# Kernel optimization log

Measured on AMD Instinct MI355X. Metric: run time of the kernel, lower is better.

Reference implementation:

```python
import jax, jax.numpy as jnp
import numpy as np

N_NODES = 50000
N_EDGES = 800000
IN_DIM = 100
HIDDEN = 16
N_CLASSES = 40


def setup_inputs() -> dict:
    key = jax.random.key(0)
    k1, k2, k3, k4, k5, k6 = jax.random.split(key, 6)
    features = jax.random.normal(k1, (N_NODES, IN_DIM), dtype=jnp.float32)
    edge_src = jax.random.randint(k2, (N_EDGES,), 0, N_NODES, dtype=jnp.int32)
    edge_dst = jax.random.randint(k3, (N_EDGES,), 0, N_NODES, dtype=jnp.int32)
    edge_vals = jax.random.uniform(k4, (N_EDGES,), dtype=jnp.float32)
    W1 = jax.random.uniform(k5, (IN_DIM, HIDDEN), dtype=jnp.float32)
    W2 = jax.random.uniform(k6, (HIDDEN, N_CLASSES), dtype=jnp.float32)
    return {"features": features, "edge_src": edge_src, "edge_dst": edge_dst,
            "edge_vals": edge_vals, "W1": W1, "W2": W2}


def _spmm(edge_src, edge_dst, edge_vals, x):
    # z = A @ x with A given as (dst, src, val) edge list; equivalent to the
    # partition-loop addmm accumulation in broadcast().
    msgs = edge_vals[:, None] * x[edge_src]            # [E, d]
    return jax.ops.segment_sum(msgs, edge_dst, num_segments=x.shape[0])


def reference(features, edge_src, edge_dst, edge_vals, W1, W2):
    h = jax.nn.relu(_spmm(edge_src, edge_dst, edge_vals, features) @ W1)  # [N, 16]
    out = _spmm(edge_src, edge_dst, edge_vals, h) @ W2                    # [N, C]
    return jax.nn.log_softmax(out, axis=1)
```

## Files before the change

### kernel.cpp

```cpp
#include <hip/hip_runtime.h>

#define N_NODES   50000
#define N_EDGES   800000
#define IN_DIM    100
#define HIDDEN    16
#define N_CLASSES 40

#define BSHIFT 6
#define NPB    64
#define NBKT   782
#define PB     256
#define EPB    3125
#define CAP    2048
#define GNODES 32

#define GROWS 64
__global__ __launch_bounds__(256) void gemm_xw1(const float* __restrict__ X,
                                                const float* __restrict__ W,
                                                float* __restrict__ Y) {
    __shared__ __align__(16) float sX[GROWS * IN_DIM];
    __shared__ __align__(16) float sW[IN_DIM * HIDDEN];
    const int tid  = threadIdx.x;
    const int row0 = blockIdx.x * GROWS;
    const int nrows = min(GROWS, N_NODES - row0);

    const float4* W4 = (const float4*)W;
    float4* sW4 = (float4*)sW;
    for (int i = tid; i < (IN_DIM * HIDDEN) / 4; i += 256) sW4[i] = W4[i];

    const float4* X4 = (const float4*)(X + (size_t)row0 * IN_DIM);
    float4* sX4 = (float4*)sX;
    const int nf4 = nrows * (IN_DIM / 4);
    for (int i = tid; i < nf4; i += 256) sX4[i] = X4[i];
    __syncthreads();

    const int r = tid >> 2;
    const int q = tid & 3;
    if (r >= nrows) return;

    float4 acc = make_float4(0.f, 0.f, 0.f, 0.f);
    const float* xr = &sX[r * IN_DIM];
#pragma unroll
    for (int k = 0; k < IN_DIM; ++k) {
        const float xk = xr[k];
        const float4 w = *(const float4*)&sW[k * HIDDEN + q * 4];
        acc.x = fmaf(xk, w.x, acc.x);
        acc.y = fmaf(xk, w.y, acc.y);
        acc.z = fmaf(xk, w.z, acc.z);
        acc.w = fmaf(xk, w.w, acc.w);
    }
    *(float4*)&Y[(size_t)(row0 + r) * HIDDEN + q * 4] = acc;
}

__global__ __launch_bounds__(512) void partition_kernel(const int* __restrict__ src,
                                                        const int* __restrict__ dst,
                                                        const float* __restrict__ val,
                                                        int* __restrict__ BTt,
                                                        int2* __restrict__ binned) {
    __shared__ int  cnt[NBKT];
    __shared__ int  lcur[NBKT];
    __shared__ int  sd[512];
    __shared__ int2 staged[EPB];

    const int tid = threadIdx.x, b = blockIdx.x;
    const int e0 = b * EPB;

    for (int k = tid; k < NBKT; k += 512) cnt[k] = 0;
    __syncthreads();
    for (int i = tid; i < EPB; i += 512)
        atomicAdd(&cnt[dst[e0 + i] >> BSHIFT], 1);
    __syncthreads();

    const int k0 = 2 * tid, k1 = 2 * tid + 1;
    const int a  = (k0 < NBKT) ? cnt[k0] : 0;
    const int bb = (k1 < NBKT) ? cnt[k1] : 0;
    const int s  = a + bb;
    sd[tid] = s;
    __syncthreads();
    for (int off = 1; off < 512; off <<= 1) {
        const int u = (tid >= off) ? sd[tid - off] : 0;
        __syncthreads();
        sd[tid] += u;
        __syncthreads();
    }
    const int excl = sd[tid] - s;
    if (k0 < NBKT) { lcur[k0] = excl;     BTt[k0 * PB + b] = excl; }
    if (k1 < NBKT) { lcur[k1] = excl + a; BTt[k1 * PB + b] = excl + a; }
    if (tid == 0)  BTt[NBKT * PB + b] = EPB;
    __syncthreads();

    for (int i = tid; i < EPB; i += 512) {
        const int e = e0 + i;
        const int d = dst[e];
        const int k = d >> BSHIFT;
        const int pos = atomicAdd(&lcur[k], 1);
        staged[pos] = make_int2(src[e] | ((d & (NPB - 1)) << 16),
                                __float_as_int(val[e]));
    }
    __syncthreads();

    for (int i = tid; i < EPB; i += 512)
        binned[e0 + i] = staged[i];
}

__global__ __launch_bounds__(256) void sort_kernel(const int* __restrict__ BTt,
                                                   const int2* __restrict__ binned,
                                                   int2* __restrict__ sorted,
                                                   int2* __restrict__ meta) {
    __shared__ int  cnt[NPB];
    __shared__ int  cur[NPB];
    __shared__ int  sTot;
    __shared__ int2 staged[CAP];

    const int tid = threadIdx.x, k = blockIdx.x;
    if (tid < NPB) cnt[tid] = 0;
    __syncthreads();

    const int rs = BTt[k * PB + tid];
    const int re = BTt[(k + 1) * PB + tid];
    const int2* rb = binned + (size_t)tid * EPB;

    for (int p = rs; p < re; ++p)
        atomicAdd(&cnt[(rb[p].x >> 16) & (NPB - 1)], 1);
    __syncthreads();

    if (tid < NPB) {
        const int v  = cnt[tid];
        const int vp = (v + 1) & ~1;
        int x = vp;
#pragma unroll
        for (int d = 1; d < 64; d <<= 1) {
            const int y = __shfl_up(x, d, 64);
            if (tid >= d) x += y;
        }
        const int excl = x - vp;
        cur[tid] = excl;
        const int node = k * NPB + tid;
        if (node < N_NODES) meta[node] = make_int2(k * CAP + excl, v);
        if (tid == NPB - 1) sTot = x;
    }
    __syncthreads();

    for (int p = rs; p < re; ++p) {
        const int2 e = rb[p];
        const int  n = (e.x >> 16) & (NPB - 1);
        const int pos = atomicAdd(&cur[n], 1);
        staged[pos] = make_int2(e.x & 0xFFFF, e.y);
    }
    __syncthreads();

    const int m = sTot;
    for (int i = tid; i < m; i += 256)
        sorted[(size_t)k * CAP + i] = staged[i];
}

template <bool RELU_OUT>
__global__ __launch_bounds__(256) void gather_spmm(const int2* __restrict__ meta,
                                                   const int2* __restrict__ sorted,
                                                   const float* __restrict__ X,
                                                   float* __restrict__ Z) {
    const int tid = threadIdx.x;
    const int g = tid >> 3, j = tid & 7;
    const int n = blockIdx.x * GNODES + g;
    if (n >= N_NODES) return;
    const int2 md = meta[n];
    const int beg = md.x, end = md.x + md.y;
    const float2* X2 = (const float2*)X;

    float2 acc = make_float2(0.f, 0.f);
    int p = beg;
    for (; p + 4 <= end; p += 4) {
        const int4 ea = *(const int4*)&sorted[p];
        const int4 eb = *(const int4*)&sorted[p + 2];
        const float2 x0 = X2[(size_t)ea.x * 8 + j];
        const float2 x1 = X2[(size_t)ea.z * 8 + j];
        const float2 x2 = X2[(size_t)eb.x * 8 + j];
        const float2 x3 = X2[(size_t)eb.z * 8 + j];
        const float v0 = __int_as_float(ea.y), v1 = __int_as_float(ea.w);
        const float v2 = __int_as_float(eb.y), v3 = __int_as_float(eb.w);
        acc.x = fmaf(v0, x0.x, acc.x); acc.y = fmaf(v0, x0.y, acc.y);
        acc.x = fmaf(v1, x1.x, acc.x); acc.y = fmaf(v1, x1.y, acc.y);
        acc.x = fmaf(v2, x2.x, acc.x); acc.y = fmaf(v2, x2.y, acc.y);
        acc.x = fmaf(v3, x3.x, acc.x); acc.y = fmaf(v3, x3.y, acc.y);
    }
    for (; p < end; ++p) {
        const int2 e = sorted[p];
        const float2 x = X2[(size_t)e.x * 8 + j];
        const float v = __int_as_float(e.y);
        acc.x = fmaf(v, x.x, acc.x); acc.y = fmaf(v, x.y, acc.y);
    }
    if (RELU_OUT) { acc.x = fmaxf(acc.x, 0.f); acc.y = fmaxf(acc.y, 0.f); }
    ((float2*)Z)[(size_t)n * 8 + j] = acc;
}

__global__ __launch_bounds__(256) void gather_out(const int2* __restrict__ meta,
                                                  const int2* __restrict__ sorted,
                                                  const float* __restrict__ X,
                                                  const float* __restrict__ W2,
                                                  float* __restrict__ out) {
    __shared__ float sW[HIDDEN * N_CLASSES];
    __shared__ float zt[GNODES * 17];
    const int tid = threadIdx.x;
    for (int i = tid; i < HIDDEN * N_CLASSES; i += 256) sW[i] = W2[i];

    const int g = tid >> 3, j = tid & 7;
    const int n = blockIdx.x * GNODES + g;

    float2 acc = make_float2(0.f, 0.f);
    if (n < N_NODES) {
        const int2 md = meta[n];
        const int beg = md.x, end = md.x + md.y;
        const float2* X2 = (const float2*)X;
        int p = beg;
        for (; p + 4 <= end; p += 4) {
            const int4 ea = *(const int4*)&sorted[p];
            const int4 eb = *(const int4*)&sorted[p + 2];
            const float2 x0 = X2[(size_t)ea.x * 8 + j];
            const float2 x1 = X2[(size_t)ea.z * 8 + j];
            const float2 x2 = X2[(size_t)eb.x * 8 + j];
            const float2 x3 = X2[(size_t)eb.z * 8 + j];
            const float v0 = __int_as_float(ea.y), v1 = __int_as_float(ea.w);
            const float v2 = __int_as_float(eb.y), v3 = __int_as_float(eb.w);
            acc.x = fmaf(v0, x0.x, acc.x); acc.y = fmaf(v0, x0.y, acc.y);
            acc.x = fmaf(v1, x1.x, acc.x); acc.y = fmaf(v1, x1.y, acc.y);
            acc.x = fmaf(v2, x2.x, acc.x); acc.y = fmaf(v2, x2.y, acc.y);
            acc.x = fmaf(v3, x3.x, acc.x); acc.y = fmaf(v3, x3.y, acc.y);
        }
        for (; p < end; ++p) {
            const int2 e = sorted[p];
            const float2 x = X2[(size_t)e.x * 8 + j];
            const float v = __int_as_float(e.y);
            acc.x = fmaf(v, x.x, acc.x); acc.y = fmaf(v, x.y, acc.y);
        }
    }
    zt[g * 17 + j * 2]     = acc.x;
    zt[g * 17 + j * 2 + 1] = acc.y;
    __syncthreads();
    if (n >= N_NODES) return;

    float z[HIDDEN];
#pragma unroll
    for (int k = 0; k < HIDDEN; ++k) z[k] = zt[g * 17 + k];

    float o[5];
#pragma unroll
    for (int i = 0; i < 5; ++i) o[i] = 0.f;
#pragma unroll
    for (int k = 0; k < HIDDEN; ++k) {
        const float zk = z[k];
#pragma unroll
        for (int i = 0; i < 5; ++i)
            o[i] = fmaf(zk, sW[k * N_CLASSES + j * 5 + i], o[i]);
    }

    float m = o[0];
#pragma unroll
    for (int i = 1; i < 5; ++i) m = fmaxf(m, o[i]);
#pragma unroll
    for (int d = 1; d < 8; d <<= 1) m = fmaxf(m, __shfl_xor(m, d, 8));
    float se = 0.f;
#pragma unroll
    for (int i = 0; i < 5; ++i) se += __expf(o[i] - m);
#pragma unroll
    for (int d = 1; d < 8; d <<= 1) se += __shfl_xor(se, d, 8);
    const float lse = m + __logf(se);

    float* orow = out + (size_t)n * N_CLASSES + j * 5;
#pragma unroll
    for (int i = 0; i < 5; ++i) orow[i] = o[i] - lse;
}

extern "C" void kernel_launch(void* const* d_in, const int* in_sizes, int n_in,
                              void* d_out, int out_size, void* d_ws, size_t ws_size,
                              hipStream_t stream) {
    const float* features = (const float*)d_in[0];
    const int*   edge_src = (const int*)d_in[1];
    const int*   edge_dst = (const int*)d_in[2];
    const float* edge_val = (const float*)d_in[3];
    const float* W1       = (const float*)d_in[4];
    const float* W2       = (const float*)d_in[5];
    float*       out      = (float*)d_out;

    char* base = (char*)d_ws;
    const size_t HNB = (size_t)N_NODES * HIDDEN * sizeof(float);
    float* y1     = (float*)(base);
    float* z1     = (float*)(base + HNB);
    int2*  binned = (int2*) (base + 2 * HNB);
    int2*  sortd  = (int2*) (base + 2 * HNB + (size_t)N_EDGES * 8);
    char*  tail   = base + 2 * HNB + (size_t)N_EDGES * 8
                         + (size_t)NBKT * CAP * 8;
    int*   BTt    = (int*) (tail);
    int2*  meta   = (int2*)(tail + (((size_t)(NBKT + 1) * PB * 4 + 255) & ~255ULL));

    partition_kernel<<<PB, 512, 0, stream>>>(edge_src, edge_dst, edge_val, BTt, binned);
    sort_kernel<<<NBKT, 256, 0, stream>>>(BTt, binned, sortd, meta);

    gemm_xw1<<<(N_NODES + GROWS - 1) / GROWS, 256, 0, stream>>>(features, W1, y1);
    gather_spmm<true><<<(N_NODES + GNODES - 1) / GNODES, 256, 0, stream>>>(meta, sortd, y1, z1);
    gather_out<<<(N_NODES + GNODES - 1) / GNODES, 256, 0, stream>>>(meta, sortd, z1, W2, out);
}
```

Baseline: 139.1 us.

## Fuse partition with XW1 GEMM and sort with first SpMM gather

Merges the edge partition and the X·W1 GEMM into one launch by splitting the grid into partition blocks and GEMM blocks, and merges the per-bucket sort with the first aggregation so it reads sorted edges straight from LDS. The partition pass now keeps edges in registers so dst/src/val are read from global memory once instead of twice. The sort kernel first copies its bucket's edges into LDS using a block-wide scan, then does counting and scattering there. This cuts five launches to three and removes a global round trip of the sorted edges, at the cost of heavier LDS use per block and one-thread-per-quarter-row gathers with unbalanced degrees.

New measurement: 125.6 us. 1.11x faster.

```diff
diff --git a/kernel.cpp b/kernel.cpp
--- a/kernel.cpp
+++ b/kernel.cpp
@@ -11,186 +11,196 @@
 #define NBKT   782
 #define PB     256
 #define EPB    3125
+#define EPT    7
 #define CAP    2048
 #define GNODES 32
-
-#define GROWS 64
-__global__ __launch_bounds__(256) void gemm_xw1(const float* __restrict__ X,
-                                                const float* __restrict__ W,
-                                                float* __restrict__ Y) {
-    __shared__ __align__(16) float sX[GROWS * IN_DIM];
-    __shared__ __align__(16) float sW[IN_DIM * HIDDEN];
-    const int tid  = threadIdx.x;
-    const int row0 = blockIdx.x * GROWS;
-    const int nrows = min(GROWS, N_NODES - row0);
-
-    const float4* W4 = (const float4*)W;
-    float4* sW4 = (float4*)sW;
-    for (int i = tid; i < (IN_DIM * HIDDEN) / 4; i += 256) sW4[i] = W4[i];
-
-    const float4* X4 = (const float4*)(X + (size_t)row0 * IN_DIM);
-    float4* sX4 = (float4*)sX;
-    const int nf4 = nrows * (IN_DIM / 4);
-    for (int i = tid; i < nf4; i += 256) sX4[i] = X4[i];
-    __syncthreads();
-
-    const int r = tid >> 2;
-    const int q = tid & 3;
-    if (r >= nrows) return;
-
-    float4 acc = make_float4(0.f, 0.f, 0.f, 0.f);
-    const float* xr = &sX[r * IN_DIM];
-#pragma unroll
-    for (int k = 0; k < IN_DIM; ++k) {
-        const float xk = xr[k];
-        const float4 w = *(const float4*)&sW[k * HIDDEN + q * 4];
-        acc.x = fmaf(xk, w.x, acc.x);
-        acc.y = fmaf(xk, w.y, acc.y);
-        acc.z = fmaf(xk, w.z, acc.z);
-        acc.w = fmaf(xk, w.w, acc.w);
-    }
-    *(float4*)&Y[(size_t)(row0 + r) * HIDDEN + q * 4] = acc;
+#define GEMMB  782
+
+#define K1_LDS 33456
+
+__global__ __launch_bounds__(512) void build_and_gemm(const int* __restrict__ src,
+                                                      const int* __restrict__ dst,
+                                                      const float* __restrict__ val,
+                                                      const float* __restrict__ X,
+                                                      const float* __restrict__ W,
+                                                      int* __restrict__ BTt,
+                                                      int2* __restrict__ binned,
+                                                      float* __restrict__ Y) {
+    __shared__ __align__(16) char smem[K1_LDS];
+    const int tid = threadIdx.x;
+
+    if (blockIdx.x < PB) {
+        int*  cnt    = (int*)smem;
+        int*  lcur   = (int*)(smem + 3200);
+        int*  sd     = (int*)(smem + 6400);
+        int2* staged = (int2*)(smem + 8448);
+        const int b = blockIdx.x, e0 = b * EPB;
+
+        for (int k = tid; k < NBKT; k += 512) cnt[k] = 0;
+        __syncthreads();
+
+        int pk[EPT], ps[EPT]; float pv[EPT];
+#pragma unroll
+        for (int q = 0; q < EPT; ++q) {
+            const int i = tid + q * 512;
+            if (i < EPB) {
+                const int e = e0 + i;
+                const int d = dst[e];
+                pk[q] = d >> BSHIFT;
+                ps[q] = src[e] | ((d & (NPB - 1)) << 16);
+                pv[q] = val[e];
+                atomicAdd(&cnt[pk[q]], 1);
+            } else pk[q] = -1;
+        }
+        __syncthreads();
+
+        const int k0 = 2 * tid, k1 = 2 * tid + 1;
+        const int a  = (k0 < NBKT) ? cnt[k0] : 0;
+        const int bb = (k1 < NBKT) ? cnt[k1] : 0;
+        const int s  = a + bb;
+        sd[tid] = s;
+        __syncthreads();
+        for (int off = 1; off < 512; off <<= 1) {
+            const int u = (tid >= off) ? sd[tid - off] : 0;
+            __syncthreads();
+            sd[tid] += u;
+            __syncthreads();
+        }
+        const int excl = sd[tid] - s;
+        if (k0 < NBKT) { lcur[k0] = excl;     BTt[k0 * PB + b] = excl; }
+        if (k1 < NBKT) { lcur[k1] = excl + a; BTt[k1 * PB + b] = excl + a; }
+        if (tid == 0)  BTt[NBKT * PB + b] = EPB;
+        __syncthreads();
+
+#pragma unroll
+        for (int q = 0; q < EPT; ++q) {
+            if (pk[q] >= 0) {
+                const int pos = atomicAdd(&lcur[pk[q]], 1);
+                staged[pos] = make_int2(ps[q], __float_as_int(pv[q]));
+            }
+        }
+        __syncthreads();
+
+        for (int i = tid; i < EPB; i += 512)
+            binned[e0 + i] = staged[i];
+    } else {
+        float* sX = (float*)smem;
+        float* sW = (float*)(smem + 25600);
+        const int b2   = blockIdx.x - PB;
+        const int row0 = b2 * 64;
+        const int nrows = min(64, N_NODES - row0);
+
+        const float4* W4 = (const float4*)W;
+        float4* sW4 = (float4*)sW;
+        for (int i = tid; i < (IN_DIM * HIDDEN) / 4; i += 512) sW4[i] = W4[i];
+        const float4* X4 = (const float4*)(X + (size_t)row0 * IN_DIM);
+        float4* sX4 = (float4*)sX;
+        const int nf4 = nrows * (IN_DIM / 4);
+        for (int i = tid; i < nf4; i += 512) sX4[i] = X4[i];
+        __syncthreads();
+
+        const int r = tid >> 3, hh = tid & 7;
+        if (r >= nrows) return;
+        float2 acc = make_float2(0.f, 0.f);
+        const float* xr = &sX[r * IN_DIM];
+#pragma unroll
+        for (int k = 0; k < IN_DIM; ++k) {
+            const float xk = xr[k];
+            const float2 w = *(const float2*)&sW[k * HIDDEN + hh * 2];
+            acc.x = fmaf(xk, w.x, acc.x);
+            acc.y = fmaf(xk, w.y, acc.y);
+        }
+        *(float2*)&Y[(size_t)(row0 + r) * HIDDEN + hh * 2] = acc;
+    }
 }
 
-__global__ __launch_bounds__(512) void partition_kernel(const int* __restrict__ src,
-                                                        const int* __restrict__ dst,
-                                                        const float* __restrict__ val,
-                                                        int* __restrict__ BTt,
-                                                        int2* __restrict__ binned) {
-    __shared__ int  cnt[NBKT];
-    __shared__ int  lcur[NBKT];
-    __shared__ int  sd[512];
-    __shared__ int2 staged[EPB];
-
-    const int tid = threadIdx.x, b = blockIdx.x;
-    const int e0 = b * EPB;
-
-    for (int k = tid; k < NBKT; k += 512) cnt[k] = 0;
-    __syncthreads();
-    for (int i = tid; i < EPB; i += 512)
-        atomicAdd(&cnt[dst[e0 + i] >> BSHIFT], 1);
-    __syncthreads();
-
-    const int k0 = 2 * tid, k1 = 2 * tid + 1;
-    const int a  = (k0 < NBKT) ? cnt[k0] : 0;
-    const int bb = (k1 < NBKT) ? cnt[k1] : 0;
-    const int s  = a + bb;
-    sd[tid] = s;
-    __syncthreads();
-    for (int off = 1; off < 512; off <<= 1) {
-        const int u = (tid >= off) ? sd[tid - off] : 0;
-        __syncthreads();
-        sd[tid] += u;
-        __syncthreads();
-    }
-    const int excl = sd[tid] - s;
-    if (k0 < NBKT) { lcur[k0] = excl;     BTt[k0 * PB + b] = excl; }
-    if (k1 < NBKT) { lcur[k1] = excl + a; BTt[k1 * PB + b] = excl + a; }
-    if (tid == 0)  BTt[NBKT * PB + b] = EPB;
-    __syncthreads();
-
-    for (int i = tid; i < EPB; i += 512) {
-        const int e = e0 + i;
-        const int d = dst[e];
-        const int k = d >> BSHIFT;
-        const int pos = atomicAdd(&lcur[k], 1);
-        staged[pos] = make_int2(src[e] | ((d & (NPB - 1)) << 16),
-                                __float_as_int(val[e]));
-    }
-    __syncthreads();
-
-    for (int i = tid; i < EPB; i += 512)
-        binned[e0 + i] = staged[i];
-}
-
-__global__ __launch_bounds__(256) void sort_kernel(const int* __restrict__ BTt,
+__global__ __launch_bounds__(256) void sort_gather(const int* __restrict__ BTt,
                                                    const int2* __restrict__ binned,
+                                                   const float* __restrict__ Xin,
                                                    int2* __restrict__ sorted,
-                                                   int2* __restrict__ meta) {
+                                                   int2* __restrict__ meta,
+                                                   float* __restrict__ Z) {
+    __shared__ int2 raw[CAP];
+    __shared__ int2 srt[CAP];
     __shared__ int  cnt[NPB];
     __shared__ int  cur[NPB];
-    __shared__ int  sTot;
-    __shared__ int2 staged[CAP];
-
+    __shared__ int  wsum[4];
     const int tid = threadIdx.x, k = blockIdx.x;
+    const int lane = tid & 63, w = tid >> 6;
+
     if (tid < NPB) cnt[tid] = 0;
-    __syncthreads();
 
     const int rs = BTt[k * PB + tid];
     const int re = BTt[(k + 1) * PB + tid];
+    const int len = re - rs;
+    int x = len;
+#pragma unroll
+    for (int d = 1; d < 64; d <<= 1) {
+        const int y = __shfl_up(x, d, 64);
+        if (lane >= d) x += y;
+    }
+    if (lane == 63) wsum[w] = x;
+    __syncthreads();
+    int add = 0;
+    for (int i = 0; i < w; ++i) add += wsum[i];
+    const int tot = wsum[0] + wsum[1] + wsum[2] + wsum[3];
+
+    int o = add + x - len;
     const int2* rb = binned + (size_t)tid * EPB;
-
-    for (int p = rs; p < re; ++p)
-        atomicAdd(&cnt[(rb[p].x >> 16) & (NPB - 1)], 1);
+    for (int p = rs; p < re; ++p, ++o) raw[o] = rb[p];
+    __syncthreads();
+
+    for (int i = tid; i < tot; i += 256)
+        atomicAdd(&cnt[(raw[i].x >> 16) & (NPB - 1)], 1);
     __syncthreads();
 
     if (tid < NPB) {
         const int v  = cnt[tid];
         const int vp = (v + 1) & ~1;
-        int x = vp;
+        int xx = vp;
 #pragma unroll
         for (int d = 1; d < 64; d <<= 1) {
-            const int y = __shfl_up(x, d, 64);
-            if (tid >= d) x += y;
-        }
-        const int excl = x - vp;
+            const int y = __shfl_up(xx, d, 64);
+            if (tid >= d) xx += y;
+        }
+        const int excl = xx - vp;
         cur[tid] = excl;
         const int node = k * NPB + tid;
         if (node < N_NODES) meta[node] = make_int2(k * CAP + excl, v);
-        if (tid == NPB - 1) sTot = x;
-    }
-    __syncthreads();
-
-    for (int p = rs; p < re; ++p) {
-        const int2 e = rb[p];
-        const int  n = (e.x >> 16) & (NPB - 1);
-        const int pos = atomicAdd(&cur[n], 1);
-        staged[pos] = make_int2(e.x & 0xFFFF, e.y);
-    }
-    __syncthreads();
-
-    const int m = sTot;
-    for (int i = tid; i < m; i += 256)
-        sorted[(size_t)k * CAP + i] = staged[i];
-}
-
-template <bool RELU_OUT>
-__global__ __launch_bounds__(256) void gather_spmm(const int2* __restrict__ meta,
-                                                   const int2* __restrict__ sorted,
-                                                   const float* __restrict__ X,
-                                                   float* __restrict__ Z) {
-    const int tid = threadIdx.x;
-    const int g = tid >> 3, j = tid & 7;
-    const int n = blockIdx.x * GNODES + g;
-    if (n >= N_NODES) return;
-    const int2 md = meta[n];
-    const int beg = md.x, end = md.x + md.y;
-    const float2* X2 = (const float2*)X;
-
-    float2 acc = make_float2(0.f, 0.f);
-    int p = beg;
-    for (; p + 4 <= end; p += 4) {
-        const int4 ea = *(const int4*)&sorted[p];
-        const int4 eb = *(const int4*)&sorted[p + 2];
-        const float2 x0 = X2[(size_t)ea.x * 8 + j];
-        const float2 x1 = X2[(size_t)ea.z * 8 + j];
-        const float2 x2 = X2[(size_t)eb.x * 8 + j];
-        const float2 x3 = X2[(size_t)eb.z * 8 + j];
-        const float v0 = __int_as_float(ea.y), v1 = __int_as_float(ea.w);
-        const float v2 = __int_as_float(eb.y), v3 = __int_as_float(eb.w);
-        acc.x = fmaf(v0, x0.x, acc.x); acc.y = fmaf(v0, x0.y, acc.y);
-        acc.x = fmaf(v1, x1.x, acc.x); acc.y = fmaf(v1, x1.y, acc.y);
-        acc.x = fmaf(v2, x2.x, acc.x); acc.y = fmaf(v2, x2.y, acc.y);
-        acc.x = fmaf(v3, x3.x, acc.x); acc.y = fmaf(v3, x3.y, acc.y);
-    }
-    for (; p < end; ++p) {
-        const int2 e = sorted[p];
-        const float2 x = X2[(size_t)e.x * 8 + j];
+        if (tid == NPB - 1) wsum[0] = xx;
+    }
+    __syncthreads();
+    const int padTot = wsum[0];
+
+    for (int i = tid; i < tot; i += 256) {
+        const int2 e = raw[i];
+        const int pos = atomicAdd(&cur[(e.x >> 16) & (NPB - 1)], 1);
+        srt[pos] = make_int2(e.x & 0xFFFF, e.y);
+    }
+    __syncthreads();
+
+    for (int i = tid; i < padTot; i += 256)
+        sorted[(size_t)k * CAP + i] = srt[i];
+
+    const int g = tid >> 2, q = tid & 3;
+    const int node = k * NPB + g;
+    if (node >= N_NODES) return;
+    const int deg = cnt[g];
+    const int beg = cur[g] - deg;
+    const float4* X4 = (const float4*)Xin;
+    float4 acc = make_float4(0.f, 0.f, 0.f, 0.f);
+    for (int p = beg; p < beg + deg; ++p) {
+        const int2 e = srt[p];
         const float v = __int_as_float(e.y);
-        acc.x = fmaf(v, x.x, acc.x); acc.y = fmaf(v, x.y, acc.y);
-    }
-    if (RELU_OUT) { acc.x = fmaxf(acc.x, 0.f); acc.y = fmaxf(acc.y, 0.f); }
-    ((float2*)Z)[(size_t)n * 8 + j] = acc;
+        const float4 xv = X4[(size_t)e.x * 4 + q];
+        acc.x = fmaf(v, xv.x, acc.x);
+        acc.y = fmaf(v, xv.y, acc.y);
+        acc.z = fmaf(v, xv.z, acc.z);
+        acc.w = fmaf(v, xv.w, acc.w);
+    }
+    acc.x = fmaxf(acc.x, 0.f); acc.y = fmaxf(acc.y, 0.f);
+    acc.z = fmaxf(acc.z, 0.f); acc.w = fmaxf(acc.w, 0.f);
+    ((float4*)Z)[(size_t)node * 4 + q] = acc;
 }
 
 __global__ __launch_bounds__(256) void gather_out(const int2* __restrict__ meta,
@@ -228,9 +238,9 @@
         }
         for (; p < end; ++p) {
             const int2 e = sorted[p];
-            const float2 x = X2[(size_t)e.x * 8 + j];
+            const float2 xv = X2[(size_t)e.x * 8 + j];
             const float v = __int_as_float(e.y);
-            acc.x = fmaf(v, x.x, acc.x); acc.y = fmaf(v, x.y, acc.y);
+            acc.x = fmaf(v, xv.x, acc.x); acc.y = fmaf(v, xv.y, acc.y);
         }
     }
     zt[g * 17 + j * 2]     = acc.x;
@@ -292,10 +302,8 @@
     int*   BTt    = (int*) (tail);
     int2*  meta   = (int2*)(tail + (((size_t)(NBKT + 1) * PB * 4 + 255) & ~255ULL));
 
-    partition_kernel<<<PB, 512, 0, stream>>>(edge_src, edge_dst, edge_val, BTt, binned);
-    sort_kernel<<<NBKT, 256, 0, stream>>>(BTt, binned, sortd, meta);
-
-    gemm_xw1<<<(N_NODES + GROWS - 1) / GROWS, 256, 0, stream>>>(features, W1, y1);
-    gather_spmm<true><<<(N_NODES + GNODES - 1) / GNODES, 256, 0, stream>>>(meta, sortd, y1, z1);
+    build_and_gemm<<<PB + GEMMB, 512, 0, stream>>>(edge_src, edge_dst, edge_val,
+                                                   features, W1, BTt, binned, y1);
+    sort_gather<<<NBKT, 256, 0, stream>>>(BTt, binned, y1, sortd, meta, z1);
     gather_out<<<(N_NODES + GNODES - 1) / GNODES, 256, 0, stream>>>(meta, sortd, z1, W2, out);
 }
```
